# Kernel tuning notes

Hardware: AMD Instinct MI355X
Metric: run time of the kernel (lower is better)

## Reference

```python
import jax, jax.numpy as jnp
import numpy as np

B, N, T, HID, HOPS = 128, 32, 50, 128, 8


def setup_inputs() -> dict:
    key = jax.random.key(0)
    k1, k2, k3, k4 = jax.random.split(key, 4)
    return {
        "node_rnn_output": jax.random.normal(k1, (B, T, HID), dtype=jnp.float32),
        "neigh_rnn_output": jax.random.normal(k2, (B, N, T, HID), dtype=jnp.float32),
        "neighbors_number": jnp.ones((B,), dtype=jnp.int32),
        "W": jax.random.normal(k3, (HOPS, HID), dtype=jnp.float32) * 0.05,
        "b": jax.random.normal(k4, (HOPS,), dtype=jnp.float32) * 0.05,
    }


def reference(node_rnn_output, neigh_rnn_output, neighbors_number, W, b):
    Bb, Tt, Hd = node_rnn_output.shape
    Nn = neigh_rnn_output.shape[1]
    # neigh_rnn_output.view(B, -1, hidden)  -> [B, N*T, H]
    neigh_r = neigh_rnn_output.reshape(Bb, Nn * Tt, Hd)
    # node_rnn_output.repeat(1, N, 1)      -> tile along time axis N times
    node_tiled = jnp.tile(node_rnn_output, (1, Nn, 1))  # [B, N*T, H]
    # elementwise guide + tiny linear projection to attention hops
    Hprod = neigh_r * node_tiled                         # [B, N*T, H]
    s1 = jnp.einsum('bnh,ah->bna', Hprod, W) + b          # [B, N*T, hops]
    # original scales every sample by sqrt(neighbors_number[0])
    scale = neighbors_number[0].astype(jnp.float32) ** 0.5
    s1 = jnp.swapaxes(s1, 1, 2) / scale                   # [B, hops, N*T]
    BA = jax.nn.softmax(s1, axis=-1)                      # [B, hops, N*T]
    # BW built from A.data (detached) in the original
    BW = jax.lax.stop_gradient(BA).sum(axis=1).reshape(Bb, Nn, Tt)
    return (BW, BA, neigh_r)
```

## Files before the change

### kernel.cpp

```cpp
#include <hip/hip_runtime.h>
#include <cmath>

namespace {

typedef float f32x4 __attribute__((ext_vector_type(4)));

constexpr int Bb   = 128;
constexpr int Nn   = 32;
constexpr int Tt   = 50;
constexpr int Hh   = 128;
constexpr int HOPS = 8;
constexpr int NT   = Nn * Tt;
constexpr int POS_PER_BLOCK = 64;
constexpr int CHUNKS = NT / POS_PER_BLOCK;

__global__ __launch_bounds__(256) void ga_s1_copy(
    const float* __restrict__ node,
    const float* __restrict__ neigh,
    const int*   __restrict__ nn,
    const float* __restrict__ W,
    const float* __restrict__ bias,
    float* __restrict__ s1g,
    float* __restrict__ neigh_r)
{
    const int lane16 = threadIdx.x & 15;
    const int group  = threadIdx.x >> 4;
    const int chunk  = blockIdx.x % CHUNKS;
    const int b      = blockIdx.x / CHUNKS;

    const float rscale = rsqrtf((float)nn[0]);

    f32x4 w0[HOPS], w1[HOPS];
    #pragma unroll
    for (int a = 0; a < HOPS; ++a) {
        const f32x4* wp = reinterpret_cast<const f32x4*>(W + a * Hh + lane16 * 8);
        w0[a] = wp[0];
        w1[a] = wp[1];
    }
    const float bl = bias[lane16 >> 1];

    const int pos0 = chunk * POS_PER_BLOCK + group;
    const size_t base = ((size_t)b * NT + pos0) * Hh + lane16 * 8;

    f32x4 nb[4][2];
    #pragma unroll
    for (int p = 0; p < 4; ++p) {
        const f32x4* np = reinterpret_cast<const f32x4*>(neigh + base + (size_t)p * 16 * Hh);
        nb[p][0] = np[0];
        nb[p][1] = np[1];
    }
    #pragma unroll
    for (int p = 0; p < 4; ++p) {
        f32x4* cp = reinterpret_cast<f32x4*>(neigh_r + base + (size_t)p * 16 * Hh);
        cp[0] = nb[p][0];
        cp[1] = nb[p][1];
    }

    #pragma unroll
    for (int p = 0; p < 4; ++p) {
        const int pos = pos0 + p * 16;
        const int t   = pos % Tt;
        const f32x4* dp = reinterpret_cast<const f32x4*>(node + ((size_t)b * Tt + t) * Hh + lane16 * 8);
        const f32x4 pr0 = nb[p][0] * dp[0];
        const f32x4 pr1 = nb[p][1] * dp[1];

        float acc[HOPS];
        #pragma unroll
        for (int a = 0; a < HOPS; ++a) {
            acc[a] = pr0[0] * w0[a][0] + pr0[1] * w0[a][1] + pr0[2] * w0[a][2] + pr0[3] * w0[a][3]
                   + pr1[0] * w1[a][0] + pr1[1] * w1[a][1] + pr1[2] * w1[a][2] + pr1[3] * w1[a][3];
        }

        const bool h8 = (lane16 & 8) != 0;
        float r[4];
        #pragma unroll
        for (int k = 0; k < 4; ++k) {
            float send = h8 ? acc[k] : acc[k + 4];
            r[k] = (h8 ? acc[k + 4] : acc[k]) + __shfl_xor(send, 8, 64);
        }
        const bool h4 = (lane16 & 4) != 0;
        float s2[2];
        #pragma unroll
        for (int k = 0; k < 2; ++k) {
            float send = h4 ? r[k] : r[k + 2];
            s2[k] = (h4 ? r[k + 2] : r[k]) + __shfl_xor(send, 4, 64);
        }
        const bool h2 = (lane16 & 2) != 0;
        float send3 = h2 ? s2[0] : s2[1];
        float u = (h2 ? s2[1] : s2[0]) + __shfl_xor(send3, 2, 64);
        u += __shfl_xor(u, 1, 64);

        if (!(lane16 & 1)) {
            s1g[((size_t)b * NT + pos) * HOPS + (lane16 >> 1)] = (u + bl) * rscale;
        }
    }
}

__global__ __launch_bounds__(256) void ga_softmax(float* __restrict__ out)
{
    float* BW = out;
    float* BA = out + Bb * NT;
    const int b   = blockIdx.x;
    const int tid = threadIdx.x;

    __shared__ float s[NT * 9];
    __shared__ float sm_m[HOPS], sm_inv[HOPS];

    const float* src = BA + (size_t)b * NT * HOPS;
    for (int idx = tid; idx < NT * HOPS; idx += 256) {
        const int nt = idx >> 3;
        const int a  = idx & 7;
        s[nt * 9 + a] = src[idx];
    }
    __syncthreads();

    const int w    = tid >> 6;
    const int lane = tid & 63;
    #pragma unroll
    for (int rep = 0; rep < 2; ++rep) {
        const int a = w * 2 + rep;
        float m = -INFINITY;
        for (int nt = lane; nt < NT; nt += 64) m = fmaxf(m, s[nt * 9 + a]);
        #pragma unroll
        for (int off = 32; off >= 1; off >>= 1) m = fmaxf(m, __shfl_xor(m, off, 64));
        float sum = 0.f;
        for (int nt = lane; nt < NT; nt += 64) sum += __expf(s[nt * 9 + a] - m);
        #pragma unroll
        for (int off = 32; off >= 1; off >>= 1) sum += __shfl_xor(sum, off, 64);
        if (lane == 0) { sm_m[a] = m; sm_inv[a] = 1.0f / sum; }
    }
    __syncthreads();

    float bw[7] = {0.f, 0.f, 0.f, 0.f, 0.f, 0.f, 0.f};
    float* bab = BA + (size_t)b * HOPS * NT;
    #pragma unroll
    for (int a = 0; a < HOPS; ++a) {
        const float m   = sm_m[a];
        const float inv = sm_inv[a];
        #pragma unroll
        for (int k = 0; k < 7; ++k) {
            const int nt = tid + k * 256;
            if (nt < NT) {
                const float v = __expf(s[nt * 9 + a] - m) * inv;
                bab[a * NT + nt] = v;
                bw[k] += v;
            }
        }
    }
    float* bwb = BW + (size_t)b * NT;
    #pragma unroll
    for (int k = 0; k < 7; ++k) {
        const int nt = tid + k * 256;
        if (nt < NT) bwb[nt] = bw[k];
    }
}

}

extern "C" void kernel_launch(void* const* d_in, const int* in_sizes, int n_in,
                              void* d_out, int out_size, void* d_ws, size_t ws_size,
                              hipStream_t stream) {
    const float* node  = (const float*)d_in[0];
    const float* neigh = (const float*)d_in[1];
    const int*   nn    = (const int*)d_in[2];
    const float* W     = (const float*)d_in[3];
    const float* bias  = (const float*)d_in[4];

    float* out     = (float*)d_out;
    float* BA      = out + Bb * NT;
    float* neigh_r = BA + Bb * HOPS * NT;

    ga_s1_copy<<<dim3(Bb * CHUNKS), dim3(256), 0, stream>>>(node, neigh, nn, W, bias, BA, neigh_r);
    ga_softmax<<<dim3(Bb), dim3(256), 0, stream>>>(out);
}
```

Baseline: 55.43 us.

## Split softmax into per-row blocks with separate BW reduction kernel

The first kernel now writes scores transposed as [B, hops, N*T] straight into the BA output, and processes 5 positions per thread instead of 4. The single 128-block softmax kernel, which staged each batch's scores in shared memory, is replaced by a 1024-block row-wise softmax that keeps values in registers. A third small kernel sums the hop rows to produce BW. This raises parallelism in the softmax phase and removes the large shared-memory staging, at the cost of an extra launch and a second pass over BA. The s1 stores become strided across hops.

```diff
diff --git a/kernel.cpp b/kernel.cpp
--- a/kernel.cpp
+++ b/kernel.cpp
@@ -11,7 +11,8 @@
 constexpr int Hh   = 128;
 constexpr int HOPS = 8;
 constexpr int NT   = Nn * Tt;
-constexpr int POS_PER_BLOCK = 64;
+constexpr int PPT  = 5;
+constexpr int POS_PER_BLOCK = 16 * PPT;
 constexpr int CHUNKS = NT / POS_PER_BLOCK;
 
 __global__ __launch_bounds__(256) void ga_s1_copy(
@@ -20,7 +21,7 @@
     const int*   __restrict__ nn,
     const float* __restrict__ W,
     const float* __restrict__ bias,
-    float* __restrict__ s1g,
+    float* __restrict__ s1T,
     float* __restrict__ neigh_r)
 {
     const int lane16 = threadIdx.x & 15;
@@ -42,22 +43,22 @@
     const int pos0 = chunk * POS_PER_BLOCK + group;
     const size_t base = ((size_t)b * NT + pos0) * Hh + lane16 * 8;
 
-    f32x4 nb[4][2];
+    f32x4 nb[PPT][2];
     #pragma unroll
-    for (int p = 0; p < 4; ++p) {
+    for (int p = 0; p < PPT; ++p) {
         const f32x4* np = reinterpret_cast<const f32x4*>(neigh + base + (size_t)p * 16 * Hh);
         nb[p][0] = np[0];
         nb[p][1] = np[1];
     }
     #pragma unroll
-    for (int p = 0; p < 4; ++p) {
+    for (int p = 0; p < PPT; ++p) {
         f32x4* cp = reinterpret_cast<f32x4*>(neigh_r + base + (size_t)p * 16 * Hh);
         cp[0] = nb[p][0];
         cp[1] = nb[p][1];
     }
 
     #pragma unroll
-    for (int p = 0; p < 4; ++p) {
+    for (int p = 0; p < PPT; ++p) {
         const int pos = pos0 + p * 16;
         const int t   = pos % Tt;
         const f32x4* dp = reinterpret_cast<const f32x4*>(node + ((size_t)b * Tt + t) * Hh + lane16 * 8);
@@ -91,68 +92,73 @@
         u += __shfl_xor(u, 1, 64);
 
         if (!(lane16 & 1)) {
-            s1g[((size_t)b * NT + pos) * HOPS + (lane16 >> 1)] = (u + bl) * rscale;
+            const int k = lane16 >> 1;
+            s1T[((size_t)b * HOPS + k) * NT + pos] = (u + bl) * rscale;
         }
     }
 }
 
-__global__ __launch_bounds__(256) void ga_softmax(float* __restrict__ out)
+__global__ __launch_bounds__(256) void ga_softmax_rows(float* __restrict__ BA)
 {
-    float* BW = out;
-    float* BA = out + Bb * NT;
-    const int b   = blockIdx.x;
-    const int tid = threadIdx.x;
+    const int a = blockIdx.x & 7;
+    const int b = blockIdx.x >> 3;
+    float* row = BA + ((size_t)b * HOPS + a) * NT;
 
-    __shared__ float s[NT * 9];
-    __shared__ float sm_m[HOPS], sm_inv[HOPS];
+    const int tid  = threadIdx.x;
+    const int wv   = tid >> 6;
+    const int lane = tid & 63;
 
-    const float* src = BA + (size_t)b * NT * HOPS;
-    for (int idx = tid; idx < NT * HOPS; idx += 256) {
-        const int nt = idx >> 3;
-        const int a  = idx & 7;
-        s[nt * 9 + a] = src[idx];
-    }
-    __syncthreads();
-
-    const int w    = tid >> 6;
-    const int lane = tid & 63;
-    #pragma unroll
-    for (int rep = 0; rep < 2; ++rep) {
-        const int a = w * 2 + rep;
-        float m = -INFINITY;
-        for (int nt = lane; nt < NT; nt += 64) m = fmaxf(m, s[nt * 9 + a]);
-        #pragma unroll
-        for (int off = 32; off >= 1; off >>= 1) m = fmaxf(m, __shfl_xor(m, off, 64));
-        float sum = 0.f;
-        for (int nt = lane; nt < NT; nt += 64) sum += __expf(s[nt * 9 + a] - m);
-        #pragma unroll
-        for (int off = 32; off >= 1; off >>= 1) sum += __shfl_xor(sum, off, 64);
-        if (lane == 0) { sm_m[a] = m; sm_inv[a] = 1.0f / sum; }
-    }
-    __syncthreads();
-
-    float bw[7] = {0.f, 0.f, 0.f, 0.f, 0.f, 0.f, 0.f};
-    float* bab = BA + (size_t)b * HOPS * NT;
-    #pragma unroll
-    for (int a = 0; a < HOPS; ++a) {
-        const float m   = sm_m[a];
-        const float inv = sm_inv[a];
-        #pragma unroll
-        for (int k = 0; k < 7; ++k) {
-            const int nt = tid + k * 256;
-            if (nt < NT) {
-                const float v = __expf(s[nt * 9 + a] - m) * inv;
-                bab[a * NT + nt] = v;
-                bw[k] += v;
-            }
-        }
-    }
-    float* bwb = BW + (size_t)b * NT;
+    float v[7];
     #pragma unroll
     for (int k = 0; k < 7; ++k) {
         const int nt = tid + k * 256;
-        if (nt < NT) bwb[nt] = bw[k];
+        v[k] = (nt < NT) ? row[nt] : -INFINITY;
     }
+
+    __shared__ float red[4];
+
+    float m = v[0];
+    #pragma unroll
+    for (int k = 1; k < 7; ++k) m = fmaxf(m, v[k]);
+    #pragma unroll
+    for (int off = 32; off >= 1; off >>= 1) m = fmaxf(m, __shfl_xor(m, off, 64));
+    if (lane == 0) red[wv] = m;
+    __syncthreads();
+    m = fmaxf(fmaxf(red[0], red[1]), fmaxf(red[2], red[3]));
+    __syncthreads();
+
+    float e[7];
+    float s = 0.f;
+    #pragma unroll
+    for (int k = 0; k < 7; ++k) {
+        const int nt = tid + k * 256;
+        e[k] = (nt < NT) ? __expf(v[k] - m) : 0.f;
+        s += e[k];
+    }
+    #pragma unroll
+    for (int off = 32; off >= 1; off >>= 1) s += __shfl_xor(s, off, 64);
+    if (lane == 0) red[wv] = s;
+    __syncthreads();
+    const float inv = 1.0f / (red[0] + red[1] + red[2] + red[3]);
+
+    #pragma unroll
+    for (int k = 0; k < 7; ++k) {
+        const int nt = tid + k * 256;
+        if (nt < NT) row[nt] = e[k] * inv;
+    }
+}
+
+__global__ __launch_bounds__(256) void ga_bw(const float* __restrict__ BA,
+                                             float* __restrict__ BW)
+{
+    const int b  = blockIdx.y;
+    const int nt = blockIdx.x * 256 + threadIdx.x;
+    if (nt >= NT) return;
+    const float* base = BA + (size_t)b * HOPS * NT + nt;
+    float s = 0.f;
+    #pragma unroll
+    for (int a = 0; a < HOPS; ++a) s += base[a * NT];
+    BW[(size_t)b * NT + nt] = s;
 }
 
 }
@@ -171,5 +177,6 @@
     float* neigh_r = BA + Bb * HOPS * NT;
 
     ga_s1_copy<<<dim3(Bb * CHUNKS), dim3(256), 0, stream>>>(node, neigh, nn, W, bias, BA, neigh_r);
-    ga_softmax<<<dim3(Bb), dim3(256), 0, stream>>>(out);
+    ga_softmax_rows<<<dim3(Bb * HOPS), dim3(256), 0, stream>>>(BA);
+    ga_bw<<<dim3((NT + 255) / 256, Bb), dim3(256), 0, stream>>>(BA, out);
 }
```

Result: faster. 52.59 us (-5.1%).
